# Performance work log

Hardware: AMD Instinct MI355X
Metric: run time of the kernel (lower is better)

## Reference

```python
import jax, jax.numpy as jnp
import numpy as np

DECAY = 0.99
EPS = 1e-05
LOSS_FACTOR = 0.1


def setup_inputs() -> dict:
    key = jax.random.key(0)
    k1, k2, k3, k4 = jax.random.split(key, 4)
    x = jax.random.normal(k1, (64, 256, 32, 32), dtype=jnp.float32)
    centroids = jax.random.normal(k2, (256, 1024), dtype=jnp.float32)
    cluster_size = jax.random.uniform(k3, (1024,), dtype=jnp.float32)
    centroids_avg = jax.random.normal(k4, (256, 1024), dtype=jnp.float32)
    return {"x": x, "centroids": centroids, "cluster_size": cluster_size,
            "centroids_avg": centroids_avg}


def _forward(x, centroids, cluster_size, centroids_avg):
    F, K = centroids.shape
    # torch: x_flat = x.transpose(-1, 1).contiguous().view(-1, n_features)
    xs = jnp.swapaxes(x, 1, -1)              # [B, W, H, C]
    flat_shape = xs.shape
    xf = xs.reshape(-1, F)                   # [N, F]
    dist = ((xf * xf).sum(1, keepdims=True)
            + (centroids * centroids).sum(0, keepdims=True)
            - 2.0 * (xf @ centroids))        # [N, K]
    ind = jnp.argmin(dist, axis=1)           # [N] nearest centroid
    # training-path EMA updates (one-hot matmuls expressed as segment sums)
    counts = jax.ops.segment_sum(jnp.ones(ind.shape, dtype=xf.dtype), ind,
                                 num_segments=K)              # [K]
    centroids_sum = jax.ops.segment_sum(xf, ind, num_segments=K).T  # [F, K]
    new_cs = DECAY * cluster_size + (1.0 - DECAY) * counts
    new_avg = DECAY * centroids_avg + (1.0 - DECAY) * centroids_sum
    n = new_cs.sum()
    cs_norm = (new_cs + EPS) / (n + K * EPS) * n
    new_centroids = new_avg / cs_norm[None, :]               # [F, K]
    # quantize with updated codebook (embedding lookup)
    xq = new_centroids.T[ind].reshape(flat_shape)            # [B, W, H, C]
    xq = jnp.swapaxes(xq, 1, -1)                             # [B, C, H, W]
    xq_st = x + jax.lax.stop_gradient(xq - x)                # straight-through
    return xq_st, xq


def reference(x, centroids, cluster_size, centroids_avg):
    out, _ = _forward(x, centroids, cluster_size, centroids_avg)
    return out
```

## Files before the change

### kernel.cpp

```cpp
#include <hip/hip_runtime.h>


#define DECAY 0.99f
#define EPSF 1e-5f
#define DELTA 0.05f

typedef _Float16 f16x8 __attribute__((ext_vector_type(8)));
typedef float f32x4 __attribute__((ext_vector_type(4)));

static __device__ __forceinline__ unsigned short h_bits(_Float16 h) {
  return __builtin_bit_cast(unsigned short, h);
}
static __device__ __forceinline__ float h_val(unsigned short u) {
  return (float)__builtin_bit_cast(_Float16, u);
}

__global__ void csq_kernel(const float* __restrict__ cent, float* __restrict__ csq) {
  int k0 = blockIdx.x * 64;
  int t = threadIdx.x;
  int kk = t & 63, cg = t >> 6;
  float s = 0.f;
  for (int c = cg; c < 256; c += 4) {
    float v = cent[(size_t)c * 1024 + k0 + kk];
    s += v * v;
  }
  __shared__ float red[4][64];
  red[cg][kk] = s;
  __syncthreads();
  if (t < 64) csq[k0 + t] = red[0][t] + red[1][t] + red[2][t] + red[3][t];
}

__global__ void centT_kernel(const float* __restrict__ cent, _Float16* __restrict__ ctp) {
  __shared__ float tl[32][33];
  int f0 = (blockIdx.x >> 5) * 32, k0 = (blockIdx.x & 31) * 32;
  int t = threadIdx.x;
#pragma unroll
  for (int i = 0; i < 4; ++i) {
    int fi = (t >> 5) + i * 8, ki = t & 31;
    tl[fi][ki] = cent[(size_t)(f0 + fi) * 1024 + k0 + ki];
  }
  __syncthreads();
#pragma unroll
  for (int i = 0; i < 4; ++i) {
    int ki = (t >> 5) + i * 8, fi = t & 31;
    int k = k0 + ki, f = f0 + fi;
    _Float16 h = (_Float16)tl[fi][ki];
    size_t idx = (size_t)(k >> 4) * 4096 + (size_t)(f >> 5) * 512 +
                 (size_t)(k & 15) * 32 + (size_t)((f >> 3) & 3) * 8 + (f & 7);
    ctp[idx] = h;
  }
}

__global__ void transpose_kernel(const float* __restrict__ x, _Float16* __restrict__ xh,
                                 _Float16* __restrict__ xl) {
  __shared__ float tile[64][65];
  int bid = blockIdx.x;
  int pt = bid & 15, ct = (bid >> 4) & 3, b = bid >> 6;
  int c0 = ct * 64, p0 = pt * 64;
  int t = threadIdx.x;
#pragma unroll
  for (int i = 0; i < 16; ++i) {
    int idx = t + i * 256;
    int ci = idx >> 6, pi = idx & 63;
    tile[ci][pi] = x[((size_t)(b * 256 + c0 + ci) << 10) + p0 + pi];
  }
  __syncthreads();
#pragma unroll
  for (int i = 0; i < 8; ++i) {
    int idx = t + i * 256;
    int pi = idx >> 5, cp = idx & 31;
    int p = p0 + pi;
    int r = ((p & 31) << 5) | (p >> 5);
    float v0 = tile[cp * 2][pi], v1 = tile[cp * 2 + 1][pi];
    _Float16 h0 = (_Float16)v0, h1 = (_Float16)v1;
    _Float16 l0 = (_Float16)(v0 - (float)h0), l1 = (_Float16)(v1 - (float)h1);
    unsigned int uh = (unsigned int)h_bits(h0) | ((unsigned int)h_bits(h1) << 16);
    unsigned int ul = (unsigned int)h_bits(l0) | ((unsigned int)h_bits(l1) << 16);
    size_t base = ((size_t)((b << 10) + r)) * 128 + ct * 32 + cp;
    ((unsigned int*)xh)[base] = uh;
    ((unsigned int*)xl)[base] = ul;
  }
}

__global__ __launch_bounds__(256, 4) void mfma_argmin_kernel(
    const _Float16* __restrict__ xh, const _Float16* __restrict__ xl,
    const _Float16* __restrict__ ctp, const float* __restrict__ csq,
    int* __restrict__ ind, int* __restrict__ flaglist,
    unsigned int* __restrict__ flagcnt, unsigned int* __restrict__ counts) {
  __shared__ _Float16 Ah[32 * 256];
  __shared__ _Float16 Al[32 * 256];
  __shared__ float csql[1024];
  __shared__ float red1[4][32], red2[4][32];
  __shared__ int redk[4][32];
  const int t = threadIdx.x;
  const int lane = t & 63, w = t >> 6;
  const int lr = lane & 15, lg = lane >> 4;
  const int n0 = blockIdx.x * 32;

#pragma unroll
  for (int i = 0; i < 4; ++i) csql[t + i * 256] = csq[t + i * 256];
#pragma unroll
  for (int i = 0; i < 4; ++i) {
    int idx = t + i * 256;
    int row = idx >> 5, c16 = (idx & 31) * 16;
    int sw = c16 ^ ((row & 7) << 4);
    *(f16x8*)((char*)Ah + row * 512 + sw) =
        *(const f16x8*)((const char*)xh + (size_t)(n0 + row) * 512 + c16);
  }
#pragma unroll
  for (int i = 0; i < 4; ++i) {
    int idx = t + i * 256;
    int row = idx >> 5, c16 = (idx & 31) * 16;
    int sw = c16 ^ ((row & 7) << 4);
    *(f16x8*)((char*)Al + row * 512 + sw) =
        *(const f16x8*)((const char*)xl + (size_t)(n0 + row) * 512 + c16);
  }
  __syncthreads();

  float b1[2][4], b2v[2][4];
  int bk[2][4];
#pragma unroll
  for (int rt = 0; rt < 2; ++rt)
#pragma unroll
    for (int rg = 0; rg < 4; ++rg) { b1[rt][rg] = 3.4e38f; b2v[rt][rg] = 3.4e38f; bk[rt][rg] = 0; }

  const int swz = (lr & 7) << 4;
  const int boff = (lr * 4 + lg) * 16;
#pragma unroll 1
  for (int ch = 0; ch < 4; ++ch) {
    const int ccb = w * 256 + ch * 64;
    const int colt0 = ccb >> 4;
    f32x4 acc[4][2];
#pragma unroll
    for (int ct = 0; ct < 4; ++ct)
#pragma unroll
      for (int rt = 0; rt < 2; ++rt) acc[ct][rt] = (f32x4){0.f, 0.f, 0.f, 0.f};

#pragma unroll 1
    for (int ks = 0; ks < 8; ++ks) {
      f16x8 bh[4];
#pragma unroll
      for (int ct = 0; ct < 4; ++ct)
        bh[ct] = *(const f16x8*)((const char*)ctp +
                                 (size_t)(colt0 + ct) * 8192 + ks * 1024 + boff);
      f16x8 ah[2], al[2];
#pragma unroll
      for (int rt = 0; rt < 2; ++rt) {
        int off = (rt * 16 + lr) * 512 + ((ks * 64 + lg * 16) ^ swz);
        ah[rt] = *(const f16x8*)((const char*)Ah + off);
        al[rt] = *(const f16x8*)((const char*)Al + off);
      }
#pragma unroll
      for (int ct = 0; ct < 4; ++ct)
#pragma unroll
        for (int rt = 0; rt < 2; ++rt) {
          acc[ct][rt] = __builtin_amdgcn_mfma_f32_16x16x32_f16(ah[rt], bh[ct], acc[ct][rt], 0, 0, 0);
          acc[ct][rt] = __builtin_amdgcn_mfma_f32_16x16x32_f16(al[rt], bh[ct], acc[ct][rt], 0, 0, 0);
        }
    }
#pragma unroll
    for (int ct = 0; ct < 4; ++ct) {
      const int col = ccb + ct * 16 + lr;
      const float cq = csql[col];
#pragma unroll
      for (int rt = 0; rt < 2; ++rt)
#pragma unroll
        for (int rg = 0; rg < 4; ++rg) {
          float d = cq - 2.f * acc[ct][rt][rg];
          if (d < b1[rt][rg]) {
            b2v[rt][rg] = b1[rt][rg];
            b1[rt][rg] = d;
            bk[rt][rg] = col;
          } else if (d < b2v[rt][rg]) {
            b2v[rt][rg] = d;
          }
        }
    }
  }

#pragma unroll
  for (int rt = 0; rt < 2; ++rt)
#pragma unroll
    for (int rg = 0; rg < 4; ++rg) {
      float v1 = b1[rt][rg], v2 = b2v[rt][rg];
      int kk = bk[rt][rg];
#pragma unroll
      for (int off = 8; off >= 1; off >>= 1) {
        float o1 = __shfl_xor(v1, off);
        int ok = __shfl_xor(kk, off);
        float o2 = __shfl_xor(v2, off);
        float nb2 = fminf(fmaxf(v1, o1), fminf(v2, o2));
        if (o1 < v1 || (o1 == v1 && ok < kk)) { v1 = o1; kk = ok; }
        v2 = nb2;
      }
      if (lr == 0) {
        int row = rt * 16 + lg * 4 + rg;
        red1[w][row] = v1;
        redk[w][row] = kk;
        red2[w][row] = v2;
      }
    }
  __syncthreads();
  if (t < 32) {
    float v1 = red1[0][t], v2 = red2[0][t];
    int kk = redk[0][t];
#pragma unroll
    for (int wi = 1; wi < 4; ++wi) {
      float o1 = red1[wi][t], o2 = red2[wi][t];
      int ok = redk[wi][t];
      float nb2 = fminf(fmaxf(v1, o1), fminf(v2, o2));
      if (o1 < v1 || (o1 == v1 && ok < kk)) { v1 = o1; kk = ok; }
      v2 = nb2;
    }
    ind[n0 + t] = kk;
    atomicAdd(&counts[kk], 1u);
    if (v2 - v1 < DELTA) {
      unsigned int p = atomicAdd(flagcnt, 1u);
      flaglist[p] = n0 + t;
    }
  }
}

__global__ __launch_bounds__(256) void fixup_kernel(
    const _Float16* __restrict__ xh, const _Float16* __restrict__ xl,
    const float* __restrict__ cent, const float* __restrict__ csq,
    const int* __restrict__ flaglist, const unsigned int* __restrict__ flagcnt,
    int* __restrict__ ind, unsigned int* __restrict__ counts) {
  const int t = threadIdx.x;
  const int nf = (int)*flagcnt;
  __shared__ float xrow[256];
  __shared__ float rv[256];
  __shared__ int rk[256];
  for (int ii = blockIdx.x; ii < nf; ii += gridDim.x) {
    __syncthreads();
    int row = flaglist[ii];
    xrow[t] = (float)xh[(size_t)row * 256 + t] + (float)xl[(size_t)row * 256 + t];
    __syncthreads();
    float a0 = 0.f, a1 = 0.f, a2 = 0.f, a3 = 0.f;
#pragma unroll 8
    for (int f = 0; f < 256; ++f) {
      float xs = xrow[f];
      const float* cr = cent + (size_t)f * 1024 + t;
      a0 += xs * cr[0];
      a1 += xs * cr[256];
      a2 += xs * cr[512];
      a3 += xs * cr[768];
    }
    float bd = csq[t] - 2.f * a0;
    int bkk = t;
    float d1 = csq[t + 256] - 2.f * a1;
    if (d1 < bd) { bd = d1; bkk = t + 256; }
    float d2 = csq[t + 512] - 2.f * a2;
    if (d2 < bd) { bd = d2; bkk = t + 512; }
    float d3 = csq[t + 768] - 2.f * a3;
    if (d3 < bd) { bd = d3; bkk = t + 768; }
    rv[t] = bd;
    rk[t] = bkk;
    __syncthreads();
    for (int off = 128; off >= 1; off >>= 1) {
      if (t < off) {
        float ov = rv[t + off];
        int ok = rk[t + off];
        if (ov < rv[t] || (ov == rv[t] && ok < rk[t])) { rv[t] = ov; rk[t] = ok; }
      }
      __syncthreads();
    }
    if (t == 0) {
      int newk = rk[0];
      int oldk = ind[row];
      if (newk != oldk) {
        ind[row] = newk;
        atomicAdd(&counts[oldk], 0xFFFFFFFFu);
        atomicAdd(&counts[newk], 1u);
      }
    }
  }
}

__global__ __launch_bounds__(64) void csnorm_scan_kernel(
    const float* __restrict__ cs, const unsigned int* __restrict__ counts,
    float* __restrict__ icn, unsigned int* __restrict__ offsets,
    unsigned int* __restrict__ cursor) {
  const int t = threadIdx.x;
  unsigned int cl[16];
  float csl[16];
  unsigned int s = 0;
  float css = 0.f;
#pragma unroll
  for (int j = 0; j < 16; ++j) {
    cl[j] = counts[t * 16 + j];
    s += cl[j];
    csl[j] = cs[t * 16 + j];
    css += csl[j];
  }
  unsigned int incl = s;
#pragma unroll
  for (int off = 1; off < 64; off <<= 1) {
    unsigned int v = __shfl_up(incl, off);
    if (t >= off) incl += v;
  }
  unsigned int run = incl - s;
  float tot = css;
#pragma unroll
  for (int off = 32; off >= 1; off >>= 1) tot += __shfl_xor(tot, off);
  const float n = DECAY * tot + (1.f - DECAY) * 65536.f;
#pragma unroll
  for (int j = 0; j < 16; ++j) {
    int k = t * 16 + j;
    offsets[k] = run;
    cursor[k] = run;
    float ncs = DECAY * csl[j] + (1.f - DECAY) * (float)cl[j];
    float csn = (ncs + EPSF) / (n + 1024.f * EPSF) * n;
    icn[k] = 1.f / csn;
    run += cl[j];
  }
  if (t == 63) offsets[1024] = run;
}

__global__ void scatter_kernel(const int* __restrict__ ind, unsigned int* __restrict__ cursor,
                               int* __restrict__ rowlist) {
  int n = blockIdx.x * 256 + threadIdx.x;
  int k = ind[n];
  unsigned int pos = atomicAdd(&cursor[k], 1u);
  rowlist[pos] = n;
}

__global__ __launch_bounds__(256) void sumflush_kernel(
    const _Float16* __restrict__ xh, const _Float16* __restrict__ xl,
    const int* __restrict__ rowlist, const int* __restrict__ ind,
    float* __restrict__ sums) {
  __shared__ int rl[64];
  __shared__ int kl[64];
  const int t = threadIdx.x;
  const int sub = t >> 6, lane = t & 63;
  const int p0 = blockIdx.x * 64;
  if (t < 64) {
    int r = rowlist[p0 + t];
    rl[t] = r;
    kl[t] = ind[r];
  }
  __syncthreads();
  float a0 = 0.f, a1 = 0.f, a2 = 0.f, a3 = 0.f;
  int curk = kl[sub * 16];
#pragma unroll
  for (int i = 0; i < 16; ++i) {
    int p = sub * 16 + i;
    int k = kl[p];
    if (k != curk) {
      float* dst = &sums[(size_t)curk * 256 + lane * 4];
      atomicAdd(&dst[0], a0);
      atomicAdd(&dst[1], a1);
      atomicAdd(&dst[2], a2);
      atomicAdd(&dst[3], a3);
      a0 = a1 = a2 = a3 = 0.f;
      curk = k;
    }
    int r = rl[p];
    uint2 vh = *(const uint2*)&((const unsigned int*)xh)[(size_t)r * 128 + lane * 2];
    uint2 vl = *(const uint2*)&((const unsigned int*)xl)[(size_t)r * 128 + lane * 2];
    a0 += h_val((unsigned short)(vh.x & 0xFFFF)) + h_val((unsigned short)(vl.x & 0xFFFF));
    a1 += h_val((unsigned short)(vh.x >> 16)) + h_val((unsigned short)(vl.x >> 16));
    a2 += h_val((unsigned short)(vh.y & 0xFFFF)) + h_val((unsigned short)(vl.y & 0xFFFF));
    a3 += h_val((unsigned short)(vh.y >> 16)) + h_val((unsigned short)(vl.y >> 16));
  }
  float* dst = &sums[(size_t)curk * 256 + lane * 4];
  atomicAdd(&dst[0], a0);
  atomicAdd(&dst[1], a1);
  atomicAdd(&dst[2], a2);
  atomicAdd(&dst[3], a3);
}

__global__ __launch_bounds__(256) void newcentT_kernel(
    const float* __restrict__ sums, const float* __restrict__ avg,
    const float* __restrict__ icn, float* __restrict__ nc) {
  __shared__ float tl[32][33];
  const int t = threadIdx.x;
  const int k0 = (blockIdx.x & 31) * 32, f0 = (blockIdx.x >> 5) * 32;
#pragma unroll
  for (int i = 0; i < 4; ++i) {
    int ki = (t >> 5) + i * 8, fi = t & 31;
    tl[ki][fi] = sums[(size_t)(k0 + ki) * 256 + f0 + fi];
  }
  __syncthreads();
#pragma unroll
  for (int i = 0; i < 4; ++i) {
    int fi = (t >> 5) + i * 8, ki = t & 31;
    size_t idx = (size_t)(f0 + fi) * 1024 + k0 + ki;
    nc[idx] = (DECAY * avg[idx] + (1.f - DECAY) * tl[ki][fi]) * icn[k0 + ki];
  }
}

__global__ void gather_kernel(const float* __restrict__ nc, const int* __restrict__ ind,
                              float* __restrict__ out) {
  __shared__ int ip[1024];
  int b = blockIdx.x >> 3;
  int cg = (blockIdx.x & 7) * 32;
  int t = threadIdx.x;
#pragma unroll
  for (int j = 0; j < 4; ++j) {
    int p = t + j * 256;
    int r = ((p & 31) << 5) | (p >> 5);
    ip[p] = ind[(b << 10) + r];
  }
  __syncthreads();
  for (int c = cg; c < cg + 32; ++c) {
    const float* row = nc + (size_t)c * 1024;
#pragma unroll
    for (int j = 0; j < 4; ++j) {
      int p = t + j * 256;
      out[((size_t)(b * 256 + c) << 10) + p] = row[ip[p]];
    }
  }
}

extern "C" void kernel_launch(void* const* d_in, const int* in_sizes, int n_in,
                              void* d_out, int out_size, void* d_ws, size_t ws_size,
                              hipStream_t stream) {
  const float* x = (const float*)d_in[0];
  const float* cent = (const float*)d_in[1];
  const float* cs = (const float*)d_in[2];
  const float* avg = (const float*)d_in[3];
  float* out = (float*)d_out;

  char* ws = (char*)d_ws;
  _Float16* xh = (_Float16*)ws;
  _Float16* xl = (_Float16*)(ws + 33554432);
  _Float16* ctp = (_Float16*)(ws + 67108864);
  float* nc = (float*)(ws + 67108864);
  unsigned int* counts = (unsigned int*)(ws + 68157440);
  unsigned int* flagcnt = (unsigned int*)(ws + 68161536);
  float* csq = (float*)(ws + 68165632);
  float* icn = (float*)(ws + 68169728);
  unsigned int* offsets = (unsigned int*)(ws + 68173824);
  unsigned int* cursor = (unsigned int*)(ws + 68182016);
  int* ind = (int*)(ws + 68186112);
  int* flaglist = (int*)(ws + 68448256);
  int* rowlist = (int*)(ws + 68448256);
  float* sums = (float*)(ws + 68710400);

  hipMemsetAsync(counts, 0, 8192, stream);
  hipMemsetAsync(sums, 0, 1048576, stream);

  csq_kernel<<<16, 256, 0, stream>>>(cent, csq);
  centT_kernel<<<256, 256, 0, stream>>>(cent, ctp);
  transpose_kernel<<<4096, 256, 0, stream>>>(x, xh, xl);
  mfma_argmin_kernel<<<2048, 256, 0, stream>>>(xh, xl, ctp, csq, ind, flaglist, flagcnt, counts);
  fixup_kernel<<<128, 256, 0, stream>>>(xh, xl, cent, csq, flaglist, flagcnt, ind, counts);
  csnorm_scan_kernel<<<1, 64, 0, stream>>>(cs, counts, icn, offsets, cursor);
  scatter_kernel<<<256, 256, 0, stream>>>(ind, cursor, rowlist);
  sumflush_kernel<<<1024, 256, 0, stream>>>(xh, xl, rowlist, ind, sums);
  newcentT_kernel<<<256, 256, 0, stream>>>(sums, avg, icn, nc);
  gather_kernel<<<512, 256, 0, stream>>>(nc, ind, out);
}
```

Measured before the change: 296.1 us.

## Drop low-half fp16 term in argmin GEMM, enlarge row tile, prefetch centroid fragments

The argmin MFMA kernel now multiplies only the high fp16 half of x against the centroids and no longer runs the residual (low) half, which halves MFMA work and the LDS traffic for x. Each block now covers 64 rows instead of 32, so every centroid fragment loaded from global memory is reused across twice as many rows. Centroid fragments are double-buffered one k-step ahead to hide load latency. The lower precision relies on the existing second-best margin flagging and fixup kernel to correct close calls, but the larger per-thread accumulator set raises register pressure, so launch bounds drop to 3 blocks per CU.

```diff
diff --git a/kernel.cpp b/kernel.cpp
--- a/kernel.cpp
+++ b/kernel.cpp
@@ -82,45 +82,36 @@
   }
 }
 
-__global__ __launch_bounds__(256, 4) void mfma_argmin_kernel(
-    const _Float16* __restrict__ xh, const _Float16* __restrict__ xl,
-    const _Float16* __restrict__ ctp, const float* __restrict__ csq,
-    int* __restrict__ ind, int* __restrict__ flaglist,
-    unsigned int* __restrict__ flagcnt, unsigned int* __restrict__ counts) {
-  __shared__ _Float16 Ah[32 * 256];
-  __shared__ _Float16 Al[32 * 256];
+__global__ __launch_bounds__(256, 3) void mfma_argmin_kernel(
+    const _Float16* __restrict__ xh, const _Float16* __restrict__ ctp,
+    const float* __restrict__ csq, int* __restrict__ ind,
+    int* __restrict__ flaglist, unsigned int* __restrict__ flagcnt,
+    unsigned int* __restrict__ counts) {
+  __shared__ _Float16 Ah[64 * 256];
   __shared__ float csql[1024];
-  __shared__ float red1[4][32], red2[4][32];
-  __shared__ int redk[4][32];
+  __shared__ float red1[4][64], red2[4][64];
+  __shared__ int redk[4][64];
   const int t = threadIdx.x;
   const int lane = t & 63, w = t >> 6;
   const int lr = lane & 15, lg = lane >> 4;
-  const int n0 = blockIdx.x * 32;
+  const int n0 = blockIdx.x * 64;
 
 #pragma unroll
   for (int i = 0; i < 4; ++i) csql[t + i * 256] = csq[t + i * 256];
 #pragma unroll
-  for (int i = 0; i < 4; ++i) {
+  for (int i = 0; i < 8; ++i) {
     int idx = t + i * 256;
     int row = idx >> 5, c16 = (idx & 31) * 16;
     int sw = c16 ^ ((row & 7) << 4);
     *(f16x8*)((char*)Ah + row * 512 + sw) =
         *(const f16x8*)((const char*)xh + (size_t)(n0 + row) * 512 + c16);
   }
-#pragma unroll
-  for (int i = 0; i < 4; ++i) {
-    int idx = t + i * 256;
-    int row = idx >> 5, c16 = (idx & 31) * 16;
-    int sw = c16 ^ ((row & 7) << 4);
-    *(f16x8*)((char*)Al + row * 512 + sw) =
-        *(const f16x8*)((const char*)xl + (size_t)(n0 + row) * 512 + c16);
-  }
-  __syncthreads();
-
-  float b1[2][4], b2v[2][4];
-  int bk[2][4];
-#pragma unroll
-  for (int rt = 0; rt < 2; ++rt)
+  __syncthreads();
+
+  float b1[4][4], b2v[4][4];
+  int bk[4][4];
+#pragma unroll
+  for (int rt = 0; rt < 4; ++rt)
 #pragma unroll
     for (int rg = 0; rg < 4; ++rg) { b1[rt][rg] = 3.4e38f; b2v[rt][rg] = 3.4e38f; bk[rt][rg] = 0; }
 
@@ -129,41 +120,51 @@
 #pragma unroll 1
   for (int ch = 0; ch < 4; ++ch) {
     const int ccb = w * 256 + ch * 64;
-    const int colt0 = ccb >> 4;
-    f32x4 acc[4][2];
+    const size_t cbase = (size_t)(ccb >> 4) * 8192 + boff;
+    f32x4 acc[4][4];
 #pragma unroll
     for (int ct = 0; ct < 4; ++ct)
 #pragma unroll
-      for (int rt = 0; rt < 2; ++rt) acc[ct][rt] = (f32x4){0.f, 0.f, 0.f, 0.f};
-
-#pragma unroll 1
-    for (int ks = 0; ks < 8; ++ks) {
-      f16x8 bh[4];
+      for (int rt = 0; rt < 4; ++rt) acc[ct][rt] = (f32x4){0.f, 0.f, 0.f, 0.f};
+
+    f16x8 pb0[4], pb1[4], ah[4];
+#pragma unroll
+    for (int ct = 0; ct < 4; ++ct)
+      pb0[ct] = *(const f16x8*)((const char*)ctp + cbase + (size_t)ct * 8192);
+#pragma unroll
+    for (int ks2 = 0; ks2 < 4; ++ks2) {
+      const int ksA = ks2 * 2, ksB = ks2 * 2 + 1;
 #pragma unroll
       for (int ct = 0; ct < 4; ++ct)
-        bh[ct] = *(const f16x8*)((const char*)ctp +
-                                 (size_t)(colt0 + ct) * 8192 + ks * 1024 + boff);
-      f16x8 ah[2], al[2];
-#pragma unroll
-      for (int rt = 0; rt < 2; ++rt) {
-        int off = (rt * 16 + lr) * 512 + ((ks * 64 + lg * 16) ^ swz);
-        ah[rt] = *(const f16x8*)((const char*)Ah + off);
-        al[rt] = *(const f16x8*)((const char*)Al + off);
+        pb1[ct] = *(const f16x8*)((const char*)ctp + cbase + (size_t)ct * 8192 + ksB * 1024);
+#pragma unroll
+      for (int rt = 0; rt < 4; ++rt)
+        ah[rt] = *(const f16x8*)((const char*)Ah + (rt * 16 + lr) * 512 + ((ksA * 64 + lg * 16) ^ swz));
+#pragma unroll
+      for (int ct = 0; ct < 4; ++ct)
+#pragma unroll
+        for (int rt = 0; rt < 4; ++rt)
+          acc[ct][rt] = __builtin_amdgcn_mfma_f32_16x16x32_f16(ah[rt], pb0[ct], acc[ct][rt], 0, 0, 0);
+      if (ks2 < 3) {
+#pragma unroll
+        for (int ct = 0; ct < 4; ++ct)
+          pb0[ct] = *(const f16x8*)((const char*)ctp + cbase + (size_t)ct * 8192 + (ksA + 2) * 1024);
       }
 #pragma unroll
+      for (int rt = 0; rt < 4; ++rt)
+        ah[rt] = *(const f16x8*)((const char*)Ah + (rt * 16 + lr) * 512 + ((ksB * 64 + lg * 16) ^ swz));
+#pragma unroll
       for (int ct = 0; ct < 4; ++ct)
 #pragma unroll
-        for (int rt = 0; rt < 2; ++rt) {
-          acc[ct][rt] = __builtin_amdgcn_mfma_f32_16x16x32_f16(ah[rt], bh[ct], acc[ct][rt], 0, 0, 0);
-          acc[ct][rt] = __builtin_amdgcn_mfma_f32_16x16x32_f16(al[rt], bh[ct], acc[ct][rt], 0, 0, 0);
-        }
+        for (int rt = 0; rt < 4; ++rt)
+          acc[ct][rt] = __builtin_amdgcn_mfma_f32_16x16x32_f16(ah[rt], pb1[ct], acc[ct][rt], 0, 0, 0);
     }
 #pragma unroll
     for (int ct = 0; ct < 4; ++ct) {
       const int col = ccb + ct * 16 + lr;
       const float cq = csql[col];
 #pragma unroll
-      for (int rt = 0; rt < 2; ++rt)
+      for (int rt = 0; rt < 4; ++rt)
 #pragma unroll
         for (int rg = 0; rg < 4; ++rg) {
           float d = cq - 2.f * acc[ct][rt][rg];
@@ -179,7 +180,7 @@
   }
 
 #pragma unroll
-  for (int rt = 0; rt < 2; ++rt)
+  for (int rt = 0; rt < 4; ++rt)
 #pragma unroll
     for (int rg = 0; rg < 4; ++rg) {
       float v1 = b1[rt][rg], v2 = b2v[rt][rg];
@@ -201,7 +202,7 @@
       }
     }
   __syncthreads();
-  if (t < 32) {
+  if (t < 64) {
     float v1 = red1[0][t], v2 = red2[0][t];
     int kk = redk[0][t];
 #pragma unroll
@@ -444,7 +445,7 @@
   csq_kernel<<<16, 256, 0, stream>>>(cent, csq);
   centT_kernel<<<256, 256, 0, stream>>>(cent, ctp);
   transpose_kernel<<<4096, 256, 0, stream>>>(x, xh, xl);
-  mfma_argmin_kernel<<<2048, 256, 0, stream>>>(xh, xl, ctp, csq, ind, flaglist, flagcnt, counts);
+  mfma_argmin_kernel<<<1024, 256, 0, stream>>>(xh, ctp, csq, ind, flaglist, flagcnt, counts);
   fixup_kernel<<<128, 256, 0, stream>>>(xh, xl, cent, csq, flaglist, flagcnt, ind, counts);
   csnorm_scan_kernel<<<1, 64, 0, stream>>>(cs, counts, icn, offsets, cursor);
   scatter_kernel<<<256, 256, 0, stream>>>(ind, cursor, rowlist);
```

Result: slower. 386.4 us (+30.5%).
